# Optimization experiments

Measured on AMD Instinct MI355X. Metric: run time of the kernel, lower is better.

## Reference

```python
import jax, jax.numpy as jnp
import numpy as np
from jax import lax

B, T, I, H = 8192, 512, 3, 25  # batch, seq_len, input_size, hidden_size


def setup_inputs() -> dict:
    key = jax.random.key(0)
    ks = jax.random.split(key, 4)
    x = jax.random.normal(ks[0], (B, T, I), dtype=jnp.float32)
    # xavier-uniform-ish scale for w_ih, orthogonal-ish (plain normal here) for w_hh
    w_ih = jax.random.normal(ks[1], (4 * H, I), dtype=jnp.float32) * 0.5
    w_hh = jax.random.normal(ks[2], (4 * H, H), dtype=jnp.float32) * 0.2
    b_ih = jnp.zeros((4 * H,), dtype=jnp.float32)
    # PyTorch init in module: forget-gate bias (second quarter) set to 1 on each bias
    b_ih = b_ih.at[H:2 * H].set(1.0)
    b_hh = jnp.zeros((4 * H,), dtype=jnp.float32)
    b_hh = b_hh.at[H:2 * H].set(1.0)
    w_lin = jax.random.normal(ks[3], (1, H), dtype=jnp.float32) * 0.3
    b_lin = jnp.zeros((1,), dtype=jnp.float32)
    return {"x": x, "w_ih": w_ih, "w_hh": w_hh, "b_ih": b_ih, "b_hh": b_hh,
            "w_lin": w_lin, "b_lin": b_lin}


def _lstm_last_h(x, w_ih, w_hh, b_ih, b_hh):
    # x: [B, T, I]; returns final hidden state h_T: [B, H]
    b = b_ih + b_hh  # [4H]
    xT = jnp.swapaxes(x, 0, 1)  # [T, B, I]

    def step(carry, x_t):
        h, c = carry
        gates = x_t @ w_ih.T + h @ w_hh.T + b  # [B, 4H]
        i, f, g, o = jnp.split(gates, 4, axis=-1)  # PyTorch gate order i,f,g,o
        i = jax.nn.sigmoid(i)
        f = jax.nn.sigmoid(f)
        g = jnp.tanh(g)
        o = jax.nn.sigmoid(o)
        c = f * c + i * g
        h = o * jnp.tanh(c)
        return (h, c), None

    h0 = jnp.zeros((x.shape[0], w_hh.shape[1]), dtype=x.dtype)
    (h, _), _ = lax.scan(step, (h0, h0), xT)
    return h


def reference(x, w_ih, w_hh, b_ih, b_hh, w_lin, b_lin):
    h_last = _lstm_last_h(x, w_ih, w_hh, b_ih, b_hh)  # [B, H]
    return h_last @ w_lin.T + b_lin  # [B, 1]
```

## Files before the change

### kernel.cpp

```cpp
#include <hip/hip_runtime.h>
#include <hip/hip_bf16.h>


#define TSTEPS 512
#define ISZ 3
#define HSZ 25
#define NW 7
#define CHUNK 256
#define TSTRIDE 40

typedef __attribute__((ext_vector_type(8))) short bf16x8;
typedef __attribute__((ext_vector_type(4))) float f32x4;
typedef __attribute__((ext_vector_type(2))) float v2f;

__device__ __forceinline__ unsigned short bf16_bits(float v) {
    return __builtin_bit_cast(unsigned short, __float2bfloat16(v));
}
__device__ __forceinline__ unsigned int pack_bf16(float lo, float hi) {
    return ((unsigned int)bf16_bits(hi) << 16) | (unsigned int)bf16_bits(lo);
}

__global__ __launch_bounds__(NW * 64) void lstm_mfma(
    const float* __restrict__ x,
    const float* __restrict__ w_ih,
    const float* __restrict__ w_hh,
    const float* __restrict__ b_ih,
    const float* __restrict__ b_hh,
    const float* __restrict__ w_lin,
    const float* __restrict__ b_lin,
    float* __restrict__ out)
{
    __shared__ uint2 xpk[CHUNK][16];
    __shared__ short hb[2][16 * TSTRIDE];
    __shared__ float outred[NW][16];

    const int tid  = threadIdx.x;
    const int w    = tid >> 6;
    const int lane = tid & 63;
    const int n    = lane & 15;
    const int q    = lane >> 4;
    const int u    = 4 * w + q;
    const bool isxw = (w == 6) && (q == 1);

    for (int i = tid; i < 2 * 16 * TSTRIDE; i += NW * 64) ((short*)hb)[i] = 0;

    auto stage = [&](int c0) {
        if (tid < 256) {
            const int bsel = tid >> 4, sub16 = tid & 15;
            const float* __restrict__ g =
                x + (size_t)(blockIdx.x * 16 + bsel) * (TSTEPS * ISZ) + c0 * ISZ;
            #pragma unroll
            for (int it = 0; it < 4; ++it) {
                const int tg = sub16 + 16 * it;
                const float4* f4 = (const float4*)(g + tg * 12);
                float4 a = f4[0], b4 = f4[1], c4 = f4[2];
                const float s[4][3] = { {a.x, a.y, a.z}, {a.w, b4.x, b4.y},
                                        {b4.z, b4.w, c4.x}, {c4.y, c4.z, c4.w} };
                #pragma unroll
                for (int uu = 0; uu < 4; ++uu) {
                    uint2 d;
                    d.x = pack_bf16(s[uu][0], s[uu][1]);
                    d.y = pack_bf16(s[uu][2], 1.0f);
                    xpk[tg * 4 + uu][bsel] = d;
                }
            }
        }
    };
    stage(0);

    bf16x8 afrag;
    #pragma unroll
    for (int j = 0; j < 8; ++j) {
        const int k = q * 8 + j;
        const int r = 16 * w + n;
        const int uu = r >> 2, g = r & 3;
        float v = 0.0f;
        if (uu < HSZ) {
            const int orow = g * HSZ + uu;
            if (k < ISZ)            v = w_ih[orow * ISZ + k];
            else if (k == ISZ)      v = b_ih[orow] + b_hh[orow];
            else if (k < 4 + HSZ)   v = w_hh[orow * HSZ + (k - 4)];
        }
        afrag[j] = (short)bf16_bits(v);
    }

    __syncthreads();
    if (isxw) *(uint2*)&hb[0][n * TSTRIDE] = xpk[0][n];
    __syncthreads();

    float c = 0.f, h = 0.f;
    const int rdoff = n * TSTRIDE + q * 8;
    const int wroff = n * TSTRIDE + 4 + u;
    const int xwoff = n * TSTRIDE;
    const float K1 = 1.442695040888963f;
    const float K2 = 2.885390081777927f;

    auto step = [&](int t, short* __restrict__ rb, short* __restrict__ wb) {
        const bf16x8 bfrag = *reinterpret_cast<const bf16x8*>(rb + rdoff);
        const f32x4 acc = __builtin_amdgcn_mfma_f32_16x16x32_bf16(
            afrag, bfrag, (f32x4){0.f, 0.f, 0.f, 0.f}, 0, 0, 0);

        v2f p01 = (v2f){acc[0], acc[1]} * (v2f){-K1, -K1};
        v2f p23 = (v2f){acc[2], acc[3]} * (v2f){-K2, -K1};
        const float e0 = __builtin_amdgcn_exp2f(p01.x);
        const float e1 = __builtin_amdgcn_exp2f(p01.y);
        const float e2 = __builtin_amdgcn_exp2f(fminf(p23.x, 126.0f));
        const float e3 = __builtin_amdgcn_exp2f(p23.y);
        v2f s02 = (v2f){e0, e2} + (v2f){1.0f, 1.0f};
        v2f s13 = (v2f){e1, e3} + (v2f){1.0f, 1.0f};
        const float f  = __builtin_amdgcn_rcpf(s13.x);
        const float ig = (1.0f - e2) * __builtin_amdgcn_rcpf(s02.x * s02.y);
        c = fmaf(f, c, ig);
        const float ec = __builtin_amdgcn_exp2f(fminf(-K2 * c, 126.0f));
        h = (1.0f - ec) * __builtin_amdgcn_rcpf(s13.y * (1.0f + ec));

        wb[wroff] = (short)bf16_bits(h);
        if (isxw) *(uint2*)&wb[xwoff] = xpk[(t + 1) & (CHUNK - 1)][n];
        __syncthreads();
    };

    #pragma unroll 1
    for (int p = 0; p < 127; ++p) {
        const int t = 2 * p;
        step(t, hb[0], hb[1]);
        step(t + 1, hb[1], hb[0]);
    }
    step(254, hb[0], hb[1]);
    stage(CHUNK);
    __syncthreads();
    step(255, hb[1], hb[0]);
    #pragma unroll 1
    for (int p = 0; p < 128; ++p) {
        const int t = 256 + 2 * p;
        step(t, hb[0], hb[1]);
        step(t + 1, hb[1], hb[0]);
    }

    const float wl = (u < HSZ) ? w_lin[u] : 0.0f;
    float v = wl * h;
    v += __shfl_xor(v, 16);
    v += __shfl_xor(v, 32);
    if (lane < 16) outred[w][lane] = v;
    __syncthreads();
    if (tid < 16) {
        float s = b_lin[0];
        #pragma unroll
        for (int k = 0; k < NW; ++k) s += outred[k][tid];
        out[blockIdx.x * 16 + tid] = s;
    }
}

extern "C" void kernel_launch(void* const* d_in, const int* in_sizes, int n_in,
                              void* d_out, int out_size, void* d_ws, size_t ws_size,
                              hipStream_t stream) {
    const float* x     = (const float*)d_in[0];
    const float* w_ih  = (const float*)d_in[1];
    const float* w_hh  = (const float*)d_in[2];
    const float* b_ih  = (const float*)d_in[3];
    const float* b_hh  = (const float*)d_in[4];
    const float* w_lin = (const float*)d_in[5];
    const float* b_lin = (const float*)d_in[6];
    float* out = (float*)d_out;

    lstm_mfma<<<8192 / 16, NW * 64, 0, stream>>>(x, w_ih, w_hh, b_ih, b_hh,
                                                 w_lin, b_lin, out);
}
```

Measured before the change: 259.2 us.

## Process two 16-sequence tiles per block to amortize per-step barrier

```diff
diff --git a/kernel.cpp b/kernel.cpp
--- a/kernel.cpp
+++ b/kernel.cpp
@@ -6,7 +6,7 @@
 #define ISZ 3
 #define HSZ 25
 #define NW 7
-#define CHUNK 256
+#define CHUNK 128
 #define TSTRIDE 40
 
 typedef __attribute__((ext_vector_type(8))) short bf16x8;
@@ -19,6 +19,9 @@
 __device__ __forceinline__ unsigned int pack_bf16(float lo, float hi) {
     return ((unsigned int)bf16_bits(hi) << 16) | (unsigned int)bf16_bits(lo);
 }
+__device__ __forceinline__ v2f rcp2(v2f v) {
+    return (v2f){__builtin_amdgcn_rcpf(v.x), __builtin_amdgcn_rcpf(v.y)};
+}
 
 __global__ __launch_bounds__(NW * 64) void lstm_mfma(
     const float* __restrict__ x,
@@ -30,9 +33,11 @@
     const float* __restrict__ b_lin,
     float* __restrict__ out)
 {
-    __shared__ uint2 xpk[CHUNK][16];
-    __shared__ short hb[2][16 * TSTRIDE];
-    __shared__ float outred[NW][16];
+    __shared__ uint2 xpkA[CHUNK][16];
+    __shared__ uint2 xpkB[CHUNK][16];
+    __shared__ short hbA[2][16 * TSTRIDE];
+    __shared__ short hbB[2][16 * TSTRIDE];
+    __shared__ float outred[NW][32];
 
     const int tid  = threadIdx.x;
     const int w    = tid >> 6;
@@ -40,17 +45,20 @@
     const int n    = lane & 15;
     const int q    = lane >> 4;
     const int u    = 4 * w + q;
-    const bool isxw = (w == 6) && (q == 1);
+    const bool isxf = (w == 3) && ((unsigned)(q - 1) < 2u);
 
-    for (int i = tid; i < 2 * 16 * TSTRIDE; i += NW * 64) ((short*)hb)[i] = 0;
+    for (int i = tid; i < 2 * 16 * TSTRIDE; i += NW * 64) {
+        ((short*)hbA)[i] = 0;
+        ((short*)hbB)[i] = 0;
+    }
 
-    auto stage = [&](int c0) {
+    auto stagepass = [&](int c0, int rowbase, uint2 (*dst)[16]) {
         if (tid < 256) {
             const int bsel = tid >> 4, sub16 = tid & 15;
             const float* __restrict__ g =
-                x + (size_t)(blockIdx.x * 16 + bsel) * (TSTEPS * ISZ) + c0 * ISZ;
+                x + (size_t)(rowbase + bsel) * (TSTEPS * ISZ) + c0 * ISZ;
             #pragma unroll
-            for (int it = 0; it < 4; ++it) {
+            for (int it = 0; it < CHUNK / 64; ++it) {
                 const int tg = sub16 + 16 * it;
                 const float4* f4 = (const float4*)(g + tg * 12);
                 float4 a = f4[0], b4 = f4[1], c4 = f4[2];
@@ -61,10 +69,14 @@
                     uint2 d;
                     d.x = pack_bf16(s[uu][0], s[uu][1]);
                     d.y = pack_bf16(s[uu][2], 1.0f);
-                    xpk[tg * 4 + uu][bsel] = d;
+                    dst[tg * 4 + uu][bsel] = d;
                 }
             }
         }
+    };
+    auto stage = [&](int c0) {
+        stagepass(c0, blockIdx.x * 32, xpkA);
+        stagepass(c0, blockIdx.x * 32 + 16, xpkB);
     };
     stage(0);
 
@@ -85,68 +97,82 @@
     }
 
     __syncthreads();
-    if (isxw) *(uint2*)&hb[0][n * TSTRIDE] = xpk[0][n];
+
+    auto xfeed = [&](int slot, int wp) {
+        if (isxf) {
+            const uint2* src = (q == 1) ? &xpkA[slot][n] : &xpkB[slot][n];
+            short*       dst = (q == 1) ? hbA[wp] : hbB[wp];
+            *(uint2*)&dst[n * TSTRIDE] = *src;
+        }
+    };
+    xfeed(0, 0);
     __syncthreads();
 
-    float c = 0.f, h = 0.f;
+    v2f c = {0.f, 0.f}, h = {0.f, 0.f};
     const int rdoff = n * TSTRIDE + q * 8;
     const int wroff = n * TSTRIDE + 4 + u;
-    const int xwoff = n * TSTRIDE;
     const float K1 = 1.442695040888963f;
     const float K2 = 2.885390081777927f;
 
-    auto step = [&](int t, short* __restrict__ rb, short* __restrict__ wb) {
-        const bf16x8 bfrag = *reinterpret_cast<const bf16x8*>(rb + rdoff);
-        const f32x4 acc = __builtin_amdgcn_mfma_f32_16x16x32_bf16(
-            afrag, bfrag, (f32x4){0.f, 0.f, 0.f, 0.f}, 0, 0, 0);
+    auto step = [&](int t, int rp, int wp) {
+        const bf16x8 bA = *reinterpret_cast<const bf16x8*>(&hbA[rp][rdoff]);
+        const bf16x8 bB = *reinterpret_cast<const bf16x8*>(&hbB[rp][rdoff]);
+        const f32x4 aA = __builtin_amdgcn_mfma_f32_16x16x32_bf16(
+            afrag, bA, (f32x4){0.f, 0.f, 0.f, 0.f}, 0, 0, 0);
+        const f32x4 aB = __builtin_amdgcn_mfma_f32_16x16x32_bf16(
+            afrag, bB, (f32x4){0.f, 0.f, 0.f, 0.f}, 0, 0, 0);
 
-        v2f p01 = (v2f){acc[0], acc[1]} * (v2f){-K1, -K1};
-        v2f p23 = (v2f){acc[2], acc[3]} * (v2f){-K2, -K1};
-        const float e0 = __builtin_amdgcn_exp2f(p01.x);
-        const float e1 = __builtin_amdgcn_exp2f(p01.y);
-        const float e2 = __builtin_amdgcn_exp2f(fminf(p23.x, 126.0f));
-        const float e3 = __builtin_amdgcn_exp2f(p23.y);
-        v2f s02 = (v2f){e0, e2} + (v2f){1.0f, 1.0f};
-        v2f s13 = (v2f){e1, e3} + (v2f){1.0f, 1.0f};
-        const float f  = __builtin_amdgcn_rcpf(s13.x);
-        const float ig = (1.0f - e2) * __builtin_amdgcn_rcpf(s02.x * s02.y);
-        c = fmaf(f, c, ig);
-        const float ec = __builtin_amdgcn_exp2f(fminf(-K2 * c, 126.0f));
-        h = (1.0f - ec) * __builtin_amdgcn_rcpf(s13.y * (1.0f + ec));
+        const v2f e0 = {__builtin_amdgcn_exp2f(-K1 * aA[0]),
+                        __builtin_amdgcn_exp2f(-K1 * aB[0])};
+        const v2f e1 = {__builtin_amdgcn_exp2f(-K1 * aA[1]),
+                        __builtin_amdgcn_exp2f(-K1 * aB[1])};
+        const v2f e2 = {__builtin_amdgcn_exp2f(fminf(-K2 * aA[2], 126.0f)),
+                        __builtin_amdgcn_exp2f(fminf(-K2 * aB[2], 126.0f))};
+        const v2f e3 = {__builtin_amdgcn_exp2f(-K1 * aA[3]),
+                        __builtin_amdgcn_exp2f(-K1 * aB[3])};
+        const v2f ff = rcp2(e1 + 1.0f);
+        const v2f ig = (1.0f - e2) * rcp2((e0 + 1.0f) * (e2 + 1.0f));
+        c = ff * c + ig;
+        const v2f ec = {__builtin_amdgcn_exp2f(fminf(-K2 * c.x, 126.0f)),
+                        __builtin_amdgcn_exp2f(fminf(-K2 * c.y, 126.0f))};
+        h = (1.0f - ec) * rcp2((e3 + 1.0f) * (1.0f + ec));
 
-        wb[wroff] = (short)bf16_bits(h);
-        if (isxw) *(uint2*)&wb[xwoff] = xpk[(t + 1) & (CHUNK - 1)][n];
+        hbA[wp][wroff] = (short)bf16_bits(h.x);
+        hbB[wp][wroff] = (short)bf16_bits(h.y);
+        xfeed((t + 1) & (CHUNK - 1), wp);
         __syncthreads();
     };
 
     #pragma unroll 1
-    for (int p = 0; p < 127; ++p) {
-        const int t = 2 * p;
-        step(t, hb[0], hb[1]);
-        step(t + 1, hb[1], hb[0]);
-    }
-    step(254, hb[0], hb[1]);
-    stage(CHUNK);
-    __syncthreads();
-    step(255, hb[1], hb[0]);
-    #pragma unroll 1
-    for (int p = 0; p < 128; ++p) {
-        const int t = 256 + 2 * p;
-        step(t, hb[0], hb[1]);
-        step(t + 1, hb[1], hb[0]);
+    for (int ch = 0; ch < 4; ++ch) {
+        const int t0 = ch * CHUNK;
+        #pragma unroll 1
+        for (int p = 0; p < 63; ++p) {
+            step(t0 + 2 * p, 0, 1);
+            step(t0 + 2 * p + 1, 1, 0);
+        }
+        step(t0 + 126, 0, 1);
+        if (ch < 3) stage((ch + 1) * CHUNK);
+        __syncthreads();
+        step(t0 + 127, 1, 0);
     }
 
     const float wl = (u < HSZ) ? w_lin[u] : 0.0f;
-    float v = wl * h;
-    v += __shfl_xor(v, 16);
-    v += __shfl_xor(v, 32);
-    if (lane < 16) outred[w][lane] = v;
+    v2f v = h * wl;
+    v.x += __shfl_xor(v.x, 16);
+    v.y += __shfl_xor(v.y, 16);
+    v.x += __shfl_xor(v.x, 32);
+    v.y += __shfl_xor(v.y, 32);
+    if (lane < 16) {
+        outred[w][lane]      = v.x;
+        outred[w][16 + lane] = v.y;
+    }
     __syncthreads();
-    if (tid < 16) {
+    if (tid < 32) {
         float s = b_lin[0];
         #pragma unroll
         for (int k = 0; k < NW; ++k) s += outred[k][tid];
-        out[blockIdx.x * 16 + tid] = s;
+        out[blockIdx.x * 32 + tid] = s;
     }
 }
 
@@ -162,6 +188,6 @@
     const float* b_lin = (const float*)d_in[6];
     float* out = (float*)d_out;
 
-    lstm_mfma<<<8192 / 16, NW * 64, 0, stream>>>(x, w_ih, w_hh, b_ih, b_hh,
+    lstm_mfma<<<8192 / 32, NW * 64, 0, stream>>>(x, w_ih, w_hh, b_ih, b_hh,
                                                  w_lin, b_lin, out);
 }
```

After: 266.8 us. 2.9% more time.

## Interleave two independent batch groups per block to hide recurrence latency

Applied to the files above, without the earlier changes.

```diff
diff --git a/kernel.cpp b/kernel.cpp
--- a/kernel.cpp
+++ b/kernel.cpp
@@ -6,8 +6,6 @@
 #define ISZ 3
 #define HSZ 25
 #define NW 7
-#define CHUNK 256
-#define TSTRIDE 40
 
 typedef __attribute__((ext_vector_type(8))) short bf16x8;
 typedef __attribute__((ext_vector_type(4))) float f32x4;
@@ -30,9 +28,9 @@
     const float* __restrict__ b_lin,
     float* __restrict__ out)
 {
-    __shared__ uint2 xpk[CHUNK][16];
-    __shared__ short hb[2][16 * TSTRIDE];
-    __shared__ float outred[NW][16];
+    __shared__ uint2 xpk[2][TSTEPS][16];
+    __shared__ short hb[2][2][512];
+    __shared__ float outred[NW][32];
 
     const int tid  = threadIdx.x;
     const int w    = tid >> 6;
@@ -40,17 +38,19 @@
     const int n    = lane & 15;
     const int q    = lane >> 4;
     const int u    = 4 * w + q;
-    const bool isxw = (w == 6) && (q == 1);
+    const bool isxfA = (w == 3) && (q == 1);
+    const bool isxfB = (w == 3) && (q == 2);
 
-    for (int i = tid; i < 2 * 16 * TSTRIDE; i += NW * 64) ((short*)hb)[i] = 0;
+    for (int i = tid; i < 2 * 2 * 512; i += NW * 64) ((short*)hb)[i] = 0;
 
-    auto stage = [&](int c0) {
-        if (tid < 256) {
-            const int bsel = tid >> 4, sub16 = tid & 15;
+    if (tid < 256) {
+        const int bsel = tid >> 4, sub16 = tid & 15;
+        #pragma unroll 1
+        for (int cch = 0; cch < 2; ++cch) {
             const float* __restrict__ g =
-                x + (size_t)(blockIdx.x * 16 + bsel) * (TSTEPS * ISZ) + c0 * ISZ;
-            #pragma unroll
-            for (int it = 0; it < 4; ++it) {
+                x + (size_t)(blockIdx.x * 32 + cch * 16 + bsel) * (TSTEPS * ISZ);
+            #pragma unroll 2
+            for (int it = 0; it < TSTEPS / 64; ++it) {
                 const int tg = sub16 + 16 * it;
                 const float4* f4 = (const float4*)(g + tg * 12);
                 float4 a = f4[0], b4 = f4[1], c4 = f4[2];
@@ -61,12 +61,11 @@
                     uint2 d;
                     d.x = pack_bf16(s[uu][0], s[uu][1]);
                     d.y = pack_bf16(s[uu][2], 1.0f);
-                    xpk[tg * 4 + uu][bsel] = d;
+                    xpk[cch][tg * 4 + uu][bsel] = d;
                 }
             }
         }
-    };
-    stage(0);
+    }
 
     bf16x8 afrag;
     #pragma unroll
@@ -85,21 +84,20 @@
     }
 
     __syncthreads();
-    if (isxw) *(uint2*)&hb[0][n * TSTRIDE] = xpk[0][n];
+    if (isxfA) *(uint2*)&hb[0][0][n * 8] = xpk[0][0][n];
+    if (isxfB) *(uint2*)&hb[1][0][n * 8] = xpk[1][0][n];
     __syncthreads();
 
-    float c = 0.f, h = 0.f;
-    const int rdoff = n * TSTRIDE + q * 8;
-    const int wroff = n * TSTRIDE + 4 + u;
-    const int xwoff = n * TSTRIDE;
+    float cA = 0.f, hA = 0.f, cB = 0.f, hB = 0.f;
+    const int rdoff = lane * 8;
+    const int kk = u + 4;
+    const int wroff = (n + 16 * (kk >> 3)) * 8 + (kk & 7);
     const float K1 = 1.442695040888963f;
     const float K2 = 2.885390081777927f;
 
-    auto step = [&](int t, short* __restrict__ rb, short* __restrict__ wb) {
-        const bf16x8 bfrag = *reinterpret_cast<const bf16x8*>(rb + rdoff);
-        const f32x4 acc = __builtin_amdgcn_mfma_f32_16x16x32_bf16(
-            afrag, bfrag, (f32x4){0.f, 0.f, 0.f, 0.f}, 0, 0, 0);
+    bf16x8 fA = *reinterpret_cast<const bf16x8*>(&hb[0][0][rdoff]);
 
+    auto act = [&](const f32x4 acc, float& c, float& h) {
         v2f p01 = (v2f){acc[0], acc[1]} * (v2f){-K1, -K1};
         v2f p23 = (v2f){acc[2], acc[3]} * (v2f){-K2, -K1};
         const float e0 = __builtin_amdgcn_exp2f(p01.x);
@@ -113,40 +111,47 @@
         c = fmaf(f, c, ig);
         const float ec = __builtin_amdgcn_exp2f(fminf(-K2 * c, 126.0f));
         h = (1.0f - ec) * __builtin_amdgcn_rcpf(s13.y * (1.0f + ec));
+    };
 
-        wb[wroff] = (short)bf16_bits(h);
-        if (isxw) *(uint2*)&wb[xwoff] = xpk[(t + 1) & (CHUNK - 1)][n];
+    auto step2 = [&](int t, int rp, int wp) {
+        bf16x8 fB = *reinterpret_cast<const bf16x8*>(&hb[1][rp][rdoff]);
+        const f32x4 aA = __builtin_amdgcn_mfma_f32_16x16x32_bf16(
+            afrag, fA, (f32x4){0.f, 0.f, 0.f, 0.f}, 0, 0, 0);
+        act(aA, cA, hA);
+        hb[0][wp][wroff] = (short)bf16_bits(hA);
+        if (isxfA) *(uint2*)&hb[0][wp][n * 8] = xpk[0][(t + 1) & (TSTEPS - 1)][n];
+        __syncthreads();
+        fA = *reinterpret_cast<const bf16x8*>(&hb[0][wp][rdoff]);
+        const f32x4 aB = __builtin_amdgcn_mfma_f32_16x16x32_bf16(
+            afrag, fB, (f32x4){0.f, 0.f, 0.f, 0.f}, 0, 0, 0);
+        act(aB, cB, hB);
+        hb[1][wp][wroff] = (short)bf16_bits(hB);
+        if (isxfB) *(uint2*)&hb[1][wp][n * 8] = xpk[1][(t + 1) & (TSTEPS - 1)][n];
         __syncthreads();
     };
 
     #pragma unroll 1
-    for (int p = 0; p < 127; ++p) {
-        const int t = 2 * p;
-        step(t, hb[0], hb[1]);
-        step(t + 1, hb[1], hb[0]);
-    }
-    step(254, hb[0], hb[1]);
-    stage(CHUNK);
-    __syncthreads();
-    step(255, hb[1], hb[0]);
-    #pragma unroll 1
-    for (int p = 0; p < 128; ++p) {
-        const int t = 256 + 2 * p;
-        step(t, hb[0], hb[1]);
-        step(t + 1, hb[1], hb[0]);
+    for (int p = 0; p < TSTEPS / 2; ++p) {
+        step2(2 * p,     0, 1);
+        step2(2 * p + 1, 1, 0);
     }
 
     const float wl = (u < HSZ) ? w_lin[u] : 0.0f;
-    float v = wl * h;
-    v += __shfl_xor(v, 16);
-    v += __shfl_xor(v, 32);
-    if (lane < 16) outred[w][lane] = v;
+    float vA = wl * hA, vB = wl * hB;
+    vA += __shfl_xor(vA, 16);
+    vB += __shfl_xor(vB, 16);
+    vA += __shfl_xor(vA, 32);
+    vB += __shfl_xor(vB, 32);
+    if (lane < 16) {
+        outred[w][lane]      = vA;
+        outred[w][16 + lane] = vB;
+    }
     __syncthreads();
-    if (tid < 16) {
+    if (tid < 32) {
         float s = b_lin[0];
         #pragma unroll
         for (int k = 0; k < NW; ++k) s += outred[k][tid];
-        out[blockIdx.x * 16 + tid] = s;
+        out[blockIdx.x * 32 + tid] = s;
     }
 }
 
@@ -162,6 +167,6 @@
     const float* b_lin = (const float*)d_in[6];
     float* out = (float*)d_out;
 
-    lstm_mfma<<<8192 / 16, NW * 64, 0, stream>>>(x, w_ih, w_hh, b_ih, b_hh,
+    lstm_mfma<<<8192 / 32, NW * 64, 0, stream>>>(x, w_ih, w_hh, b_ih, b_hh,
                                                  w_lin, b_lin, out);
 }
```

New measurement: 304.6 us. 17.5% more time.

## Run each 16-sequence LSTM tile in a single wave with register-held state

Applied to the files above, without the earlier changes.

```diff
diff --git a/kernel.cpp b/kernel.cpp
--- a/kernel.cpp
+++ b/kernel.cpp
@@ -5,13 +5,11 @@
 #define TSTEPS 512
 #define ISZ 3
 #define HSZ 25
-#define NW 7
-#define CHUNK 256
-#define TSTRIDE 40
+#define NF 7
 
 typedef __attribute__((ext_vector_type(8))) short bf16x8;
 typedef __attribute__((ext_vector_type(4))) float f32x4;
-typedef __attribute__((ext_vector_type(2))) float v2f;
+typedef __attribute__((ext_vector_type(4))) int i32x4;
 
 __device__ __forceinline__ unsigned short bf16_bits(float v) {
     return __builtin_bit_cast(unsigned short, __float2bfloat16(v));
@@ -20,7 +18,7 @@
     return ((unsigned int)bf16_bits(hi) << 16) | (unsigned int)bf16_bits(lo);
 }
 
-__global__ __launch_bounds__(NW * 64) void lstm_mfma(
+__global__ __launch_bounds__(64) void lstm_wave(
     const float* __restrict__ x,
     const float* __restrict__ w_ih,
     const float* __restrict__ w_hh,
@@ -30,124 +28,124 @@
     const float* __restrict__ b_lin,
     float* __restrict__ out)
 {
-    __shared__ uint2 xpk[CHUNK][16];
-    __shared__ short hb[2][16 * TSTRIDE];
-    __shared__ float outred[NW][16];
+    __shared__ short hb[2][512];
 
-    const int tid  = threadIdx.x;
-    const int w    = tid >> 6;
-    const int lane = tid & 63;
-    const int n    = lane & 15;
-    const int q    = lane >> 4;
-    const int u    = 4 * w + q;
-    const bool isxw = (w == 6) && (q == 1);
+    const int lane = threadIdx.x;
+    const int n = lane & 15;
+    const int q = lane >> 4;
+    const int b0 = blockIdx.x * 16;
 
-    for (int i = tid; i < 2 * 16 * TSTRIDE; i += NW * 64) ((short*)hb)[i] = 0;
-
-    auto stage = [&](int c0) {
-        if (tid < 256) {
-            const int bsel = tid >> 4, sub16 = tid & 15;
-            const float* __restrict__ g =
-                x + (size_t)(blockIdx.x * 16 + bsel) * (TSTEPS * ISZ) + c0 * ISZ;
-            #pragma unroll
-            for (int it = 0; it < 4; ++it) {
-                const int tg = sub16 + 16 * it;
-                const float4* f4 = (const float4*)(g + tg * 12);
-                float4 a = f4[0], b4 = f4[1], c4 = f4[2];
-                const float s[4][3] = { {a.x, a.y, a.z}, {a.w, b4.x, b4.y},
-                                        {b4.z, b4.w, c4.x}, {c4.y, c4.z, c4.w} };
-                #pragma unroll
-                for (int uu = 0; uu < 4; ++uu) {
-                    uint2 d;
-                    d.x = pack_bf16(s[uu][0], s[uu][1]);
-                    d.y = pack_bf16(s[uu][2], 1.0f);
-                    xpk[tg * 4 + uu][bsel] = d;
-                }
-            }
-        }
-    };
-    stage(0);
-
-    bf16x8 afrag;
-    #pragma unroll
-    for (int j = 0; j < 8; ++j) {
-        const int k = q * 8 + j;
-        const int r = 16 * w + n;
-        const int uu = r >> 2, g = r & 3;
-        float v = 0.0f;
-        if (uu < HSZ) {
-            const int orow = g * HSZ + uu;
-            if (k < ISZ)            v = w_ih[orow * ISZ + k];
-            else if (k == ISZ)      v = b_ih[orow] + b_hh[orow];
-            else if (k < 4 + HSZ)   v = w_hh[orow * HSZ + (k - 4)];
-        }
-        afrag[j] = (short)bf16_bits(v);
-    }
-
-    __syncthreads();
-    if (isxw) *(uint2*)&hb[0][n * TSTRIDE] = xpk[0][n];
-    __syncthreads();
-
-    float c = 0.f, h = 0.f;
-    const int rdoff = n * TSTRIDE + q * 8;
-    const int wroff = n * TSTRIDE + 4 + u;
-    const int xwoff = n * TSTRIDE;
     const float K1 = 1.442695040888963f;
     const float K2 = 2.885390081777927f;
 
-    auto step = [&](int t, short* __restrict__ rb, short* __restrict__ wb) {
-        const bf16x8 bfrag = *reinterpret_cast<const bf16x8*>(rb + rdoff);
-        const f32x4 acc = __builtin_amdgcn_mfma_f32_16x16x32_bf16(
-            afrag, bfrag, (f32x4){0.f, 0.f, 0.f, 0.f}, 0, 0, 0);
+    ((int4*)hb)[lane]      = (int4){0, 0, 0, 0};
+    ((int4*)hb)[64 + lane] = (int4){0, 0, 0, 0};
 
-        v2f p01 = (v2f){acc[0], acc[1]} * (v2f){-K1, -K1};
-        v2f p23 = (v2f){acc[2], acc[3]} * (v2f){-K2, -K1};
-        const float e0 = __builtin_amdgcn_exp2f(p01.x);
-        const float e1 = __builtin_amdgcn_exp2f(p01.y);
-        const float e2 = __builtin_amdgcn_exp2f(fminf(p23.x, 126.0f));
-        const float e3 = __builtin_amdgcn_exp2f(p23.y);
-        v2f s02 = (v2f){e0, e2} + (v2f){1.0f, 1.0f};
-        v2f s13 = (v2f){e1, e3} + (v2f){1.0f, 1.0f};
-        const float f  = __builtin_amdgcn_rcpf(s13.x);
-        const float ig = (1.0f - e2) * __builtin_amdgcn_rcpf(s02.x * s02.y);
-        c = fmaf(f, c, ig);
-        const float ec = __builtin_amdgcn_exp2f(fminf(-K2 * c, 126.0f));
-        h = (1.0f - ec) * __builtin_amdgcn_rcpf(s13.y * (1.0f + ec));
+    bf16x8 afrag[NF];
+    #pragma unroll
+    for (int m = 0; m < NF; ++m) {
+        #pragma unroll
+        for (int j = 0; j < 8; ++j) {
+            const int k = q * 8 + j;
+            const int r = 16 * m + n;
+            const int uu = r >> 2, g = r & 3;
+            float v = 0.0f;
+            if (uu < HSZ) {
+                const int orow = g * HSZ + uu;
+                if (k < ISZ)            v = w_ih[orow * ISZ + k];
+                else if (k == ISZ)      v = b_ih[orow] + b_hh[orow];
+                else if (k < 4 + HSZ)   v = w_hh[orow * HSZ + (k - 4)];
+                v *= (g == 2) ? -K2 : -K1;
+            }
+            afrag[m][j] = (short)bf16_bits(v);
+        }
+    }
 
-        wb[wroff] = (short)bf16_bits(h);
-        if (isxw) *(uint2*)&wb[xwoff] = xpk[(t + 1) & (CHUNK - 1)][n];
-        __syncthreads();
+    float cst[NF], hst[NF];
+    #pragma unroll
+    for (int m = 0; m < NF; ++m) { cst[m] = 0.f; hst[m] = 0.f; }
+
+    const int rdoff = lane * 8;
+    int woff[NF];
+    #pragma unroll
+    for (int m = 0; m < NF; ++m) {
+        const int kw = 4 * m + q + 4;
+        woff[m] = (kw >> 3) * 128 + n * 8 + (kw & 7);
+    }
+
+    const float* __restrict__ xg = x + (size_t)(b0 + n) * (TSTEPS * ISZ);
+    float4 xc0 = ((const float4*)xg)[0];
+    float4 xc1 = ((const float4*)xg)[1];
+    float4 xc2 = ((const float4*)xg)[2];
+    float4 xn0, xn1, xn2;
+
+    __builtin_amdgcn_wave_barrier();
+
+    auto step = [&](int rp, float x0, float x1, float x2) {
+        const int wp = rp ^ 1;
+        bf16x8 frag = *(const bf16x8*)&hb[rp][rdoff];
+        i32x4 fi = __builtin_bit_cast(i32x4, frag);
+        const int px0 = (int)pack_bf16(x0, x1);
+        const int px1 = (int)pack_bf16(x2, 1.0f);
+        fi[0] = (q == 0) ? px0 : fi[0];
+        fi[1] = (q == 0) ? px1 : fi[1];
+        frag = __builtin_bit_cast(bf16x8, fi);
+
+        f32x4 acc[NF];
+        #pragma unroll
+        for (int m = 0; m < NF; ++m)
+            acc[m] = __builtin_amdgcn_mfma_f32_16x16x32_bf16(
+                afrag[m], frag, (f32x4){0.f, 0.f, 0.f, 0.f}, 0, 0, 0);
+
+        #pragma unroll
+        for (int m = 0; m < NF; ++m) {
+            const float e0 = __builtin_amdgcn_exp2f(acc[m][0]);
+            const float e1 = __builtin_amdgcn_exp2f(acc[m][1]);
+            const float e2 = __builtin_amdgcn_exp2f(fminf(acc[m][2], 126.0f));
+            const float e3 = __builtin_amdgcn_exp2f(acc[m][3]);
+            const float f  = __builtin_amdgcn_rcpf(1.0f + e1);
+            const float ig = (1.0f - e2) *
+                __builtin_amdgcn_rcpf((1.0f + e0) * (1.0f + e2));
+            cst[m] = fmaf(f, cst[m], ig);
+            const float ec = __builtin_amdgcn_exp2f(fminf(-K2 * cst[m], 126.0f));
+            hst[m] = (1.0f - ec) *
+                __builtin_amdgcn_rcpf((1.0f + e3) * (1.0f + ec));
+            hb[wp][woff[m]] = (short)bf16_bits(hst[m]);
+        }
+        __builtin_amdgcn_wave_barrier();
     };
 
     #pragma unroll 1
-    for (int p = 0; p < 127; ++p) {
-        const int t = 2 * p;
-        step(t, hb[0], hb[1]);
-        step(t + 1, hb[1], hb[0]);
-    }
-    step(254, hb[0], hb[1]);
-    stage(CHUNK);
-    __syncthreads();
-    step(255, hb[1], hb[0]);
-    #pragma unroll 1
-    for (int p = 0; p < 128; ++p) {
-        const int t = 256 + 2 * p;
-        step(t, hb[0], hb[1]);
-        step(t + 1, hb[1], hb[0]);
+    for (int g = 0; g < 128; g += 2) {
+        const float* __restrict__ p1 =
+            xg + (size_t)((g + 1 < 128 ? g + 1 : 127) * 12);
+        xn0 = ((const float4*)p1)[0];
+        xn1 = ((const float4*)p1)[1];
+        xn2 = ((const float4*)p1)[2];
+        step(0, xc0.x, xc0.y, xc0.z);
+        step(1, xc0.w, xc1.x, xc1.y);
+        step(0, xc1.z, xc1.w, xc2.x);
+        step(1, xc2.y, xc2.z, xc2.w);
+        const float* __restrict__ p2 =
+            xg + (size_t)((g + 2 < 128 ? g + 2 : 127) * 12);
+        xc0 = ((const float4*)p2)[0];
+        xc1 = ((const float4*)p2)[1];
+        xc2 = ((const float4*)p2)[2];
+        step(0, xn0.x, xn0.y, xn0.z);
+        step(1, xn0.w, xn1.x, xn1.y);
+        step(0, xn1.z, xn1.w, xn2.x);
+        step(1, xn2.y, xn2.z, xn2.w);
     }
 
-    const float wl = (u < HSZ) ? w_lin[u] : 0.0f;
-    float v = wl * h;
+    float v = 0.f;
+    #pragma unroll
+    for (int m = 0; m < NF; ++m) {
+        const int u = 4 * m + q;
+        if (u < HSZ) v = fmaf(w_lin[u], hst[m], v);
+    }
     v += __shfl_xor(v, 16);
     v += __shfl_xor(v, 32);
-    if (lane < 16) outred[w][lane] = v;
-    __syncthreads();
-    if (tid < 16) {
-        float s = b_lin[0];
-        #pragma unroll
-        for (int k = 0; k < NW; ++k) s += outred[k][tid];
-        out[blockIdx.x * 16 + tid] = s;
-    }
+    if (q == 0) out[b0 + n] = v + b_lin[0];
 }
 
 extern "C" void kernel_launch(void* const* d_in, const int* in_sizes, int n_in,
@@ -162,6 +160,6 @@
     const float* b_lin = (const float*)d_in[6];
     float* out = (float*)d_out;
 
-    lstm_mfma<<<8192 / 16, NW * 64, 0, stream>>>(x, w_ih, w_hh, b_ih, b_hh,
-                                                 w_lin, b_lin, out);
+    lstm_wave<<<8192 / 16, 64, 0, stream>>>(x, w_ih, w_hh, b_ih, b_hh,
+                                            w_lin, b_lin, out);
 }
```

New measurement: 362.5 us. +39.8%, slower.
